# Optimization experiments

Hardware: AMD Instinct MI355X
Metric: run time of the kernel (lower is better)

The kernel has to match this reference:

```python
import jax, jax.numpy as jnp
import numpy as np

NU, NV, NF = 100000, 50000, 5000
D = 64
S, EUV = 5, 500000
EUF, EVF, EFU, EFV = 1000000, 500000, 1000000, 500000


def _spmm(rows, cols, vals, x, n_out):
    # COO sparse @ dense: out[r] += v * x[c]
    return jax.ops.segment_sum(vals[:, None] * x[cols], rows, num_segments=n_out)


def setup_inputs() -> dict:
    key = jax.random.key(0)
    ks = iter(jax.random.split(key, 32))
    f32 = jnp.float32
    inp = {
        'x_u': jax.random.normal(next(ks), (NU, D), f32),
        'x_v': jax.random.normal(next(ks), (NV, D), f32),
        'x_f': jax.random.normal(next(ks), (NF, D), f32),
    }
    for w in ['W_u_uv', 'W_v_uv', 'W_f2u', 'W_f2v', 'W_u2f', 'W_v2f']:
        inp[w] = jax.random.normal(next(ks), (D, D), f32) * (1.0 / np.sqrt(D))
    def edges(name, shape, n_row, n_col):
        inp[name + '_rows'] = jax.random.randint(next(ks), shape, 0, n_row, jnp.int32)
        inp[name + '_cols'] = jax.random.randint(next(ks), shape, 0, n_col, jnp.int32)
        inp[name + '_vals'] = jax.random.uniform(next(ks), shape, f32)
    edges('uv', (S, EUV), NU, NV)
    edges('vu', (S, EUV), NV, NU)
    edges('uf', (EUF,), NU, NF)
    edges('vf', (EVF,), NV, NF)
    edges('fu', (EFU,), NF, NU)
    edges('fv', (EFV,), NF, NV)
    return inp


def reference(x_u, x_v, x_f, W_u_uv, W_v_uv, W_f2u, W_f2v, W_u2f, W_v2f,
              uv_rows, uv_cols, uv_vals, vu_rows, vu_cols, vu_vals,
              uf_rows, uf_cols, uf_vals, vf_rows, vf_cols, vf_vals,
              fu_rows, fu_cols, fu_vals, fv_rows, fv_cols, fv_vals):
    nu, nv, nf = x_u.shape[0], x_v.shape[0], x_f.shape[0]
    # dense feature transforms (dropout=0 -> identity)
    u2f = x_u @ W_u2f
    v2f = x_v @ W_v2f
    f2u = x_f @ W_f2u
    f2v = x_f @ W_f2v
    tmp_u = x_u @ W_u_uv
    tmp_v = x_v @ W_v_uv
    # sum over rating supports == one segment_sum over flattened edges
    msg_u = _spmm(uv_rows.reshape(-1), uv_cols.reshape(-1), uv_vals.reshape(-1), tmp_v, nu)
    msg_v = _spmm(vu_rows.reshape(-1), vu_cols.reshape(-1), vu_vals.reshape(-1), tmp_u, nv)
    msg_u = msg_u + _spmm(uf_rows, uf_cols, uf_vals, f2u, nu)
    msg_v = msg_v + _spmm(vf_rows, vf_cols, vf_vals, f2v, nv)
    msg_f = _spmm(fu_rows, fu_cols, fu_vals, u2f, nf) + _spmm(fv_rows, fv_cols, fv_vals, v2f, nf)
    return jax.nn.relu(msg_u), jax.nn.relu(msg_v), jax.nn.relu(msg_f)
```

## Files before the change

kernel.cpp:

```cpp
#include <hip/hip_runtime.h>


#define TDIM 64
#define EPB  4096
#define STCAP 10240

struct Rel {
    const int* rows; const int* cols; const float* vals;
    int n, chunk0, boff, shift, srcflag, eoff, coladd;
};
struct RelPack { Rel r[6]; };

struct TPack {
    const float* X[3]; const float* W1[3]; const float* W2[3];
    unsigned short* Y1[3]; unsigned short* Y2[3];
    int N[3]; int c0[3];
};

struct FSPack {
    int c0A[3], cntA[3], offA[3];
    int c0B[3], cntB[3], offB[3];
};

struct GatherPack {
    const unsigned* srcA[3]; const unsigned* srcB[3];
    int n0, n1;
};

__device__ __forceinline__ unsigned short f2bf(float f) {
    union { float f; unsigned u; } c; c.f = f;
    unsigned r = c.u + 0x7FFFu + ((c.u >> 16) & 1u);
    return (unsigned short)(r >> 16);
}
__device__ __forceinline__ float bflo(unsigned x) { return __uint_as_float(x << 16); }
__device__ __forceinline__ float bfhi(unsigned x) { return __uint_as_float(x & 0xFFFF0000u); }
__device__ __forceinline__ float pval(unsigned p) {
    return __uint_as_float((p & 0x7FFFu) << 16);
}

__global__ __launch_bounds__(256) void transform_fused_kernel(TPack T)
{
    __shared__ float xsT[64 * 68];
    __shared__ float w1s[64 * 64];
    __shared__ float w2s[64 * 64];

    int t = 0;
    if ((int)blockIdx.x >= T.c0[1]) t = 1;
    if ((int)blockIdx.x >= T.c0[2]) t = 2;
    const float* __restrict__ X  = T.X[t];
    const float* __restrict__ W1 = T.W1[t];
    const float* __restrict__ W2 = T.W2[t];
    unsigned short* __restrict__ Y1 = T.Y1[t];
    unsigned short* __restrict__ Y2 = T.Y2[t];
    const int N    = T.N[t];
    const int row0 = (blockIdx.x - T.c0[t]) * 64;
    const int tid  = threadIdx.x;

    for (int i = tid * 4; i < 4096; i += 256 * 4) {
        *(float4*)&w1s[i] = *(const float4*)&W1[i];
        *(float4*)&w2s[i] = *(const float4*)&W2[i];
    }
    {
        const int r  = tid >> 2;
        const int c0 = (tid & 3) * 16;
        const int gr = row0 + r;
        #pragma unroll
        for (int cc = 0; cc < 16; cc += 4) {
            const int c = c0 + cc;
            float4 v = make_float4(0.f, 0.f, 0.f, 0.f);
            if (gr < N) v = *(const float4*)&X[(size_t)gr * TDIM + c];
            xsT[(c + 0) * 68 + r] = v.x;
            xsT[(c + 1) * 68 + r] = v.y;
            xsT[(c + 2) * 68 + r] = v.z;
            xsT[(c + 3) * 68 + r] = v.w;
        }
    }
    __syncthreads();

    const int tx = tid & 15;
    const int ty = tid >> 4;
    float a1[4][4] = {{0.f}}, a2[4][4] = {{0.f}};

    #pragma unroll 8
    for (int k = 0; k < 64; ++k) {
        const float4 xv = *(const float4*)&xsT[k * 68 + ty * 4];
        const float4 w1 = *(const float4*)&w1s[k * 64 + tx * 4];
        const float4 w2 = *(const float4*)&w2s[k * 64 + tx * 4];
        const float xr[4] = {xv.x, xv.y, xv.z, xv.w};
        const float c1[4] = {w1.x, w1.y, w1.z, w1.w};
        const float c2[4] = {w2.x, w2.y, w2.z, w2.w};
        #pragma unroll
        for (int r = 0; r < 4; ++r)
            #pragma unroll
            for (int c = 0; c < 4; ++c) {
                a1[r][c] = fmaf(xr[r], c1[c], a1[r][c]);
                a2[r][c] = fmaf(xr[r], c2[c], a2[r][c]);
            }
    }
    #pragma unroll
    for (int r = 0; r < 4; ++r) {
        const int gr = row0 + ty * 4 + r;
        if (gr < N) {
            ushort4 o1, o2;
            o1.x = f2bf(a1[r][0]); o1.y = f2bf(a1[r][1]);
            o1.z = f2bf(a1[r][2]); o1.w = f2bf(a1[r][3]);
            o2.x = f2bf(a2[r][0]); o2.y = f2bf(a2[r][1]);
            o2.z = f2bf(a2[r][2]); o2.w = f2bf(a2[r][3]);
            ((ushort4*)Y1)[(size_t)gr * 16 + tx] = o1;
            ((ushort4*)Y2)[(size_t)gr * 16 + tx] = o2;
        }
    }
}

__device__ __forceinline__ int find_rel(const RelPack& P, int chunk) {
    int ri = 0;
    if (chunk >= P.r[1].chunk0) ri = 1;
    if (chunk >= P.r[2].chunk0) ri = 2;
    if (chunk >= P.r[3].chunk0) ri = 3;
    if (chunk >= P.r[4].chunk0) ri = 4;
    if (chunk >= P.r[5].chunk0) ri = 5;
    return ri;
}

__global__ __launch_bounds__(512) void bucketize_cm_kernel(
    RelPack P, unsigned* __restrict__ pay, unsigned char* __restrict__ binb,
    int* __restrict__ localStart, int* __restrict__ bucketTotal, int NB)
{
    __shared__ int cnt[1536];
    __shared__ int sh[512];
    __shared__ unsigned stage_pay[EPB];
    __shared__ unsigned char stage_bin[EPB];

    const int tid   = threadIdx.x;
    const int chunk = blockIdx.x;
    for (int t = tid; t < NB; t += 512) cnt[t] = 0;
    __syncthreads();

    const int ri = find_rel(P, chunk);
    const Rel M = P.r[ri];
    const int i0    = (chunk - M.chunk0) * EPB;
    const int rbase = M.eoff + i0;
    const int count = min(EPB, M.n - i0);

    const int mask = (1 << M.shift) - 1;
    const unsigned sf = (unsigned)M.srcflag;

    int      m_[EPB / 512];
    unsigned x_[EPB / 512];
    #pragma unroll
    for (int k = 0; k < EPB / 512; ++k) {
        const int i = i0 + tid + k * 512;
        m_[k] = -1;
        if (i < M.n) {
            const int row = M.rows[i];
            const int b   = M.boff + (row >> M.shift);
            m_[k] = (b << 8) | (row & mask);
            x_[k] = (unsigned)M.cols[i] + (unsigned)M.coladd;
            atomicAdd(&cnt[b], 1);
        }
    }
    __syncthreads();

    int myv[3]; int lsum = 0;
    #pragma unroll
    for (int j = 0; j < 3; ++j) {
        const int idx = tid * 3 + j;
        myv[j] = (idx < NB) ? cnt[idx] : 0;
        lsum += myv[j];
    }
    sh[tid] = lsum;
    __syncthreads();
    for (int off = 1; off < 512; off <<= 1) {
        const int x = (tid >= off) ? sh[tid - off] : 0;
        __syncthreads();
        sh[tid] += x;
        __syncthreads();
    }
    int prefix = tid ? sh[tid - 1] : 0;
    const size_t lb = (size_t)chunk * (NB + 1);
    #pragma unroll
    for (int j = 0; j < 3; ++j) {
        const int idx = tid * 3 + j;
        if (idx < NB) {
            localStart[lb + idx] = prefix;
            if (myv[j]) atomicAdd(&bucketTotal[idx], myv[j]);
            cnt[idx] = prefix;
        } else if (idx == NB) {
            localStart[lb + NB] = prefix;
        }
        prefix += myv[j];
    }
    __syncthreads();

    #pragma unroll
    for (int k = 0; k < EPB / 512; ++k) {
        if (m_[k] >= 0) {
            const int i   = i0 + tid + k * 512;
            const int b   = m_[k] >> 8;
            const int pos = atomicAdd(&cnt[b], 1);
            stage_pay[pos] = (x_[k] << 15) | ((unsigned)f2bf(M.vals[i]) & 0x7FFFu);
            stage_bin[pos] = (unsigned char)(((m_[k] & 255) << 1) | sf);
        }
    }
    __syncthreads();

    #pragma unroll
    for (int k = 0; k < EPB / 512; ++k) {
        const int j = tid + k * 512;
        if (j < count) pay[rbase + j] = stage_pay[j];
    }
    {
        const int nfull = count >> 2;
        unsigned* bout = (unsigned*)(binb + rbase);
        const unsigned* bsrc = (const unsigned*)stage_bin;
        for (int j = tid; j < nfull; j += 512) bout[j] = bsrc[j];
        if (tid < (count & 3)) binb[rbase + nfull * 4 + tid] = stage_bin[nfull * 4 + tid];
    }
}

__global__ __launch_bounds__(256) void transpose_ls_kernel(
    const int* __restrict__ src, int* __restrict__ dst, int rows, int cols)
{
    __shared__ int tile[32][33];
    const int c0 = blockIdx.x * 32;
    const int r0 = blockIdx.y * 32;
    const int tx = threadIdx.x & 31;
    const int ty = threadIdx.x >> 5;
    #pragma unroll
    for (int k = 0; k < 32; k += 8) {
        const int r = r0 + ty + k, c = c0 + tx;
        if (r < rows && c < cols) tile[ty + k][tx] = src[(size_t)r * cols + c];
    }
    __syncthreads();
    #pragma unroll
    for (int k = 0; k < 32; k += 8) {
        const int c = c0 + ty + k, r = r0 + tx;
        if (c < cols && r < rows) dst[(size_t)c * rows + r] = tile[tx][ty + k];
    }
}

__global__ __launch_bounds__(256) void bscan_kernel(
    const int* __restrict__ bucketTotal, int* __restrict__ bbase, int NB)
{
    __shared__ int sh[256];
    __shared__ int carry;
    const int t = threadIdx.x;
    if (t == 0) carry = 0;
    __syncthreads();
    for (int b0 = 0; b0 < NB; b0 += 256) {
        const int idx = b0 + t;
        const int c = (idx < NB) ? bucketTotal[idx] : 0;
        sh[t] = c;
        __syncthreads();
        for (int off = 1; off < 256; off <<= 1) {
            const int x = (t >= off) ? sh[t - off] : 0;
            __syncthreads();
            sh[t] += x;
            __syncthreads();
        }
        const int cbase = carry;
        if (idx < NB) bbase[idx] = cbase + sh[t] - c;
        __syncthreads();
        if (t == 0) carry = cbase + sh[255];
        __syncthreads();
    }
    if (t == 0) bbase[NB] = carry;
}

__global__ __launch_bounds__(512) void finesort_kernel(
    const unsigned* __restrict__ pay, const unsigned char* __restrict__ binb,
    const int* __restrict__ TL, const int* __restrict__ bbase,
    FSPack F, int* __restrict__ p2, unsigned* __restrict__ arena,
    int nbU, int nbV, int NU, int NV, int NF, int NB, int ntot_rows,
    int nchunksTot)
{
    __shared__ int cnt[512];
    __shared__ int sh[512];
    __shared__ int runS[1024], runE[1024];
    __shared__ unsigned stage[STCAP];

    const int b   = blockIdx.x;
    const int tid = threadIdx.x;

    int t, lb, rowbase;
    if (b < nbU)              { t = 0; lb = b;              rowbase = 0; }
    else if (b < nbU + nbV)   { t = 1; lb = b - nbU;        rowbase = NU; }
    else                      { t = 2; lb = b - nbU - nbV;  rowbase = NU + NV; }
    const int shift     = (t == 2) ? 5 : 7;
    const int Ntype     = (t == 0) ? NU : (t == 1) ? NV : NF;
    const int row_start = lb << shift;
    const int nrows     = min(1 << shift, Ntype - row_start);
    const int nbins     = (1 << shift) * 2;
    const int grow0     = rowbase + row_start;

    const int nA = F.cntA[t], nB_ = F.cntB[t];
    const int nRuns = nA + nB_;

    const int* __restrict__ TLb  = TL + (size_t)b * nchunksTot;
    const int* __restrict__ TLb1 = TL + (size_t)(b + 1) * nchunksTot;
    for (int i = tid; i < nRuns; i += 512) {
        int ci, base;
        if (i < nA) { ci = F.c0A[t] + i;        base = F.offA[t] + i * EPB; }
        else        { int k = i - nA;
                      ci = F.c0B[t] + k;        base = F.offB[t] + k * EPB; }
        runS[i] = base + TLb[ci];
        runE[i] = base + TLb1[ci];
    }
    if (tid < nbins) cnt[tid] = 0;
    __syncthreads();

    const int s = bbase[b];
    const int e = bbase[b + 1];
    const bool staged = (e - s) <= STCAP;
    const int grp = tid >> 4;
    const int gl  = tid & 15;

    for (int ridx = grp; ridx < nRuns; ridx += 32) {
        const int rs = runS[ridx], re = runE[ridx];
        for (int j = rs + gl; j < re; j += 16) {
            atomicAdd(&cnt[binb[j]], 1);
        }
    }
    __syncthreads();

    const int v = (tid < nbins) ? cnt[tid] : 0;
    sh[tid] = v;
    __syncthreads();
    for (int off = 1; off < 512; off <<= 1) {
        const int x = (tid >= off) ? sh[tid - off] : 0;
        __syncthreads();
        sh[tid] += x;
        __syncthreads();
    }
    const int excl = sh[tid] - v;
    if (tid < nbins) cnt[tid] = staged ? excl : (s + excl);
    if (tid < nrows * 2) p2[2 * grow0 + tid] = s + excl;
    if (b == NB - 1 && tid == 0) p2[2 * ntot_rows] = e;
    __syncthreads();

    if (staged) {
        for (int ridx = grp; ridx < nRuns; ridx += 32) {
            const int rs = runS[ridx], re = runE[ridx];
            for (int j = rs + gl; j < re; j += 16) {
                const int pos = atomicAdd(&cnt[binb[j]], 1);
                stage[pos] = pay[j];
            }
        }
        __syncthreads();
        const int seglen = e - s;
        for (int j = tid; j < seglen; j += 512) arena[s + j] = stage[j];
    } else {
        for (int ridx = grp; ridx < nRuns; ridx += 32) {
            const int rs = runS[ridx], re = runE[ridx];
            for (int j = rs + gl; j < re; j += 16) {
                const int pos = atomicAdd(&cnt[binb[j]], 1);
                arena[pos] = pay[j];
            }
        }
    }
}

__device__ __forceinline__ void accum_seg(
    const unsigned* __restrict__ src, const unsigned* __restrict__ arena,
    const int s, const int e, const int g, const int li4,
    float (&acc)[8])
{
    if (s >= e) return;
    const int nb = (e - s + 7) >> 3;
    const unsigned* __restrict__ srcp = src + li4;

    unsigned x0[4], x1[4], x2[4], x3[4];
    float w0, w1, w2, w3;

    auto issue = [&](int j, unsigned* x, float& w) {
        const int idx = j + g;
        const bool ok = idx < e;
        const unsigned cv = arena[ok ? idx : s];
        w = ok ? pval(cv) : 0.f;
        const uint4 xv = *(const uint4*)&srcp[(cv >> 15) * 32u];
        x[0] = xv.x; x[1] = xv.y; x[2] = xv.z; x[3] = xv.w;
    };
    auto fmab = [&](const unsigned* x, float w) {
        #pragma unroll
        for (int q = 0; q < 4; ++q) {
            acc[2 * q]     = fmaf(w, bflo(x[q]), acc[2 * q]);
            acc[2 * q + 1] = fmaf(w, bfhi(x[q]), acc[2 * q + 1]);
        }
    };

    issue(s,      x0, w0);
    issue(s + 8,  x1, w1);
    issue(s + 16, x2, w2);
    issue(s + 24, x3, w3);
    __builtin_amdgcn_sched_barrier(0);

    int k = 0;
    for (;;) {
        fmab(x0, w0);
        if (k + 4 < nb) issue(s + (k + 4) * 8, x0, w0);
        __builtin_amdgcn_sched_barrier(0);
        if (++k >= nb) break;
        fmab(x1, w1);
        if (k + 4 < nb) issue(s + (k + 4) * 8, x1, w1);
        __builtin_amdgcn_sched_barrier(0);
        if (++k >= nb) break;
        fmab(x2, w2);
        if (k + 4 < nb) issue(s + (k + 4) * 8, x2, w2);
        __builtin_amdgcn_sched_barrier(0);
        if (++k >= nb) break;
        fmab(x3, w3);
        if (k + 4 < nb) issue(s + (k + 4) * 8, x3, w3);
        __builtin_amdgcn_sched_barrier(0);
        if (++k >= nb) break;
    }
}

__global__ __launch_bounds__(256) void gather_all_kernel(
    const int* __restrict__ p2, const unsigned* __restrict__ arena,
    GatherPack G, float* __restrict__ out, int nrow_total)
{
    const int gid  = (blockIdx.x * 256 + threadIdx.x) >> 6;
    const int lane = threadIdx.x & 63;
    const int g    = lane >> 3;
    const int li   = lane & 7;
    const int li4  = li * 4;
    if (gid >= nrow_total) return;
    const int wid = nrow_total - 1 - gid;

    int seg = 0;
    if (wid >= G.n1)      seg = 2;
    else if (wid >= G.n0) seg = 1;
    seg = __builtin_amdgcn_readfirstlane(seg);

    const int pa = __builtin_amdgcn_readfirstlane(p2[2 * wid]);
    const int pe = __builtin_amdgcn_readfirstlane(p2[2 * wid + 2]);

    float acc[8];
    #pragma unroll
    for (int k = 0; k < 8; ++k) acc[k] = 0.f;

    if (seg < 2) {
        accum_seg(G.srcA[seg], arena, pa, pe, g, li4, acc);
    } else {
        const int pm = __builtin_amdgcn_readfirstlane(p2[2 * wid + 1]);
        accum_seg(G.srcA[2], arena, pa, pm, g, li4, acc);
        accum_seg(G.srcB[2], arena, pm, pe, g, li4, acc);
    }

    #pragma unroll
    for (int k = 0; k < 8; ++k) {
        acc[k] += __shfl_xor(acc[k], 8, 64);
        acc[k] += __shfl_xor(acc[k], 16, 64);
        acc[k] += __shfl_xor(acc[k], 32, 64);
    }

    if (g == 0) {
        float4 o0, o1;
        o0.x = fmaxf(acc[0], 0.f); o0.y = fmaxf(acc[1], 0.f);
        o0.z = fmaxf(acc[2], 0.f); o0.w = fmaxf(acc[3], 0.f);
        o1.x = fmaxf(acc[4], 0.f); o1.y = fmaxf(acc[5], 0.f);
        o1.z = fmaxf(acc[6], 0.f); o1.w = fmaxf(acc[7], 0.f);
        float4* dst = (float4*)(out + (size_t)wid * 64 + li * 8);
        dst[0] = o0;
        dst[1] = o1;
    }
}

extern "C" void kernel_launch(void* const* d_in, const int* in_sizes, int n_in,
                              void* d_out, int out_size, void* d_ws, size_t ws_size,
                              hipStream_t stream)
{
    const float* x_u    = (const float*)d_in[0];
    const float* x_v    = (const float*)d_in[1];
    const float* x_f    = (const float*)d_in[2];
    const float* W_u_uv = (const float*)d_in[3];
    const float* W_v_uv = (const float*)d_in[4];
    const float* W_f2u  = (const float*)d_in[5];
    const float* W_f2v  = (const float*)d_in[6];
    const float* W_u2f  = (const float*)d_in[7];
    const float* W_v2f  = (const float*)d_in[8];

    const int* rows_[6] = {(const int*)d_in[9],  (const int*)d_in[12],
                           (const int*)d_in[15], (const int*)d_in[18],
                           (const int*)d_in[21], (const int*)d_in[24]};
    const int* cols_[6] = {(const int*)d_in[10], (const int*)d_in[13],
                           (const int*)d_in[16], (const int*)d_in[19],
                           (const int*)d_in[22], (const int*)d_in[25]};
    const float* vals_[6] = {(const float*)d_in[11], (const float*)d_in[14],
                             (const float*)d_in[17], (const float*)d_in[20],
                             (const float*)d_in[23], (const float*)d_in[26]};

    const int NU = in_sizes[0] / TDIM;
    const int NV = in_sizes[1] / TDIM;
    const int NF = in_sizes[2] / TDIM;
    const int E_[6] = {in_sizes[9], in_sizes[12], in_sizes[15],
                       in_sizes[18], in_sizes[21], in_sizes[24]};

    const int nbU = (NU + 127) >> 7;
    const int nbV = (NV + 127) >> 7;
    const int nbF = (NF + 31) >> 5;
    const int NB  = nbU + nbV + nbF;
    const int ntot_rows = NU + NV + NF;

    const int boff_[6]   = {0, nbU, 0, nbU, nbU + nbV, nbU + nbV};
    const int shift_[6]  = {7, 7, 7, 7, 5, 5};
    const int sflag_[6]  = {0, 0, 1, 1, 0, 1};
    const int coladd_[6] = {0, 0, NV, NU, 0, 0};

    size_t etot = 0;
    int eoff_[6];
    for (int r = 0; r < 6; ++r) { eoff_[r] = (int)etot; etot += (size_t)E_[r]; }

    RelPack P;
    int nchunks = 0;
    int relchunks[6];
    for (int r = 0; r < 6; ++r) {
        P.r[r].rows = rows_[r]; P.r[r].cols = cols_[r]; P.r[r].vals = vals_[r];
        P.r[r].n = E_[r]; P.r[r].chunk0 = nchunks;
        P.r[r].boff = boff_[r]; P.r[r].shift = shift_[r]; P.r[r].srcflag = sflag_[r];
        P.r[r].eoff = eoff_[r]; P.r[r].coladd = coladd_[r];
        relchunks[r] = (E_[r] + EPB - 1) / EPB;
        nchunks += relchunks[r];
    }

    char* wsb = (char*)d_ws;
    size_t o = 0;
    auto alloc = [&](size_t bytes) {
        char* p = wsb + o;
        o = (o + bytes + 15) & ~(size_t)15;
        return p;
    };
    unsigned short* utab = (unsigned short*)alloc(((size_t)NV + NF) * TDIM * 2);
    unsigned short* vtab = (unsigned short*)alloc(((size_t)NU + NF) * TDIM * 2);
    unsigned short* u2f  = (unsigned short*)alloc((size_t)NU * TDIM * 2);
    unsigned short* v2f  = (unsigned short*)alloc((size_t)NV * TDIM * 2);
    unsigned short* tmp_v = utab;
    unsigned short* f2u   = utab + (size_t)NV * TDIM;
    unsigned short* tmp_u = vtab;
    unsigned short* f2v   = vtab + (size_t)NU * TDIM;
    int* localStart  = (int*)alloc((size_t)nchunks * (NB + 1) * 4);
    int* TL          = (int*)alloc((size_t)(NB + 1) * nchunks * 4);
    int* bucketTotal = (int*)alloc((size_t)NB * 4);
    int* bbase       = (int*)alloc((size_t)(NB + 1) * 4);
    int* p2          = (int*)alloc((size_t)(2 * ntot_rows + 1) * 4);
    unsigned* pay        = (unsigned*)alloc(etot * 4);
    unsigned char* binb  = (unsigned char*)alloc(etot);
    unsigned* arena      = (unsigned*)alloc(etot * 4);
    (void)ws_size;

    TPack T;
    T.X[0] = x_u; T.W1[0] = W_u_uv; T.W2[0] = W_u2f; T.Y1[0] = tmp_u; T.Y2[0] = u2f; T.N[0] = NU;
    T.X[1] = x_v; T.W1[1] = W_v_uv; T.W2[1] = W_v2f; T.Y1[1] = tmp_v; T.Y2[1] = v2f; T.N[1] = NV;
    T.X[2] = x_f; T.W1[2] = W_f2u;  T.W2[2] = W_f2v; T.Y1[2] = f2u;  T.Y2[2] = f2v; T.N[2] = NF;
    T.c0[0] = 0;
    T.c0[1] = (NU + 63) / 64;
    T.c0[2] = T.c0[1] + (NV + 63) / 64;
    const int tchunks = T.c0[2] + (NF + 63) / 64;
    transform_fused_kernel<<<tchunks, 256, 0, stream>>>(T);

    hipMemsetAsync(bucketTotal, 0, (size_t)NB * sizeof(int), stream);
    bucketize_cm_kernel<<<nchunks, 512, 0, stream>>>(P, pay, binb, localStart, bucketTotal, NB);
    bscan_kernel<<<1, 256, 0, stream>>>(bucketTotal, bbase, NB);
    {
        dim3 tgrid((NB + 1 + 31) / 32, (nchunks + 31) / 32);
        transpose_ls_kernel<<<tgrid, 256, 0, stream>>>(localStart, TL, nchunks, NB + 1);
    }

    FSPack F;
    const int Arel[3] = {0, 1, 4}, Brel[3] = {2, 3, 5};
    for (int t = 0; t < 3; ++t) {
        F.c0A[t] = P.r[Arel[t]].chunk0; F.cntA[t] = relchunks[Arel[t]]; F.offA[t] = eoff_[Arel[t]];
        F.c0B[t] = P.r[Brel[t]].chunk0; F.cntB[t] = relchunks[Brel[t]]; F.offB[t] = eoff_[Brel[t]];
    }
    finesort_kernel<<<NB, 512, 0, stream>>>(
        pay, binb, TL, bbase, F, p2, arena, nbU, nbV, NU, NV, NF, NB, ntot_rows, nchunks);

    GatherPack G;
    G.srcA[0] = (const unsigned*)utab;  G.srcB[0] = (const unsigned*)utab;
    G.srcA[1] = (const unsigned*)vtab;  G.srcB[1] = (const unsigned*)vtab;
    G.srcA[2] = (const unsigned*)u2f;   G.srcB[2] = (const unsigned*)v2f;
    G.n0 = NU; G.n1 = NU + NV;

    gather_all_kernel<<<(ntot_rows + 3) / 4, 256, 0, stream>>>(
        p2, arena, G, (float*)d_out, ntot_rows);
}
```

Measured before the change: 512.5 us.

## Shrink local-start tables to 16-bit, fuse bucket scan into transpose, retune finesort groups

Stores per-chunk bucket offsets as 16-bit values, since counts within a 4096-edge chunk fit, which halves the localStart/TL traffic in the bucketize, transpose and finesort kernels. The single-block bucket prefix scan is merged into block (0,0) of the transpose kernel to drop one launch. The payload packing moves into the first pass so the vals array is read once, and finesort now uses 4-lane groups over 128 runs instead of 16-lane groups over 32. The folded scan serialises work inside one transpose block, and the narrower groups change the memory access pattern of the sort.

```diff
diff --git a/kernel.cpp b/kernel.cpp
--- a/kernel.cpp
+++ b/kernel.cpp
@@ -124,7 +124,8 @@
 
 __global__ __launch_bounds__(512) void bucketize_cm_kernel(
     RelPack P, unsigned* __restrict__ pay, unsigned char* __restrict__ binb,
-    int* __restrict__ localStart, int* __restrict__ bucketTotal, int NB)
+    unsigned short* __restrict__ localStart, int* __restrict__ bucketTotal,
+    int NB)
 {
     __shared__ int cnt[1536];
     __shared__ int sh[512];
@@ -155,7 +156,8 @@
             const int row = M.rows[i];
             const int b   = M.boff + (row >> M.shift);
             m_[k] = (b << 8) | (row & mask);
-            x_[k] = (unsigned)M.cols[i] + (unsigned)M.coladd;
+            const unsigned colp = (unsigned)M.cols[i] + (unsigned)M.coladd;
+            x_[k] = (colp << 15) | ((unsigned)f2bf(M.vals[i]) & 0x7FFFu);
             atomicAdd(&cnt[b], 1);
         }
     }
@@ -182,11 +184,11 @@
     for (int j = 0; j < 3; ++j) {
         const int idx = tid * 3 + j;
         if (idx < NB) {
-            localStart[lb + idx] = prefix;
+            localStart[lb + idx] = (unsigned short)prefix;
             if (myv[j]) atomicAdd(&bucketTotal[idx], myv[j]);
             cnt[idx] = prefix;
         } else if (idx == NB) {
-            localStart[lb + NB] = prefix;
+            localStart[lb + NB] = (unsigned short)prefix;
         }
         prefix += myv[j];
     }
@@ -195,10 +197,9 @@
     #pragma unroll
     for (int k = 0; k < EPB / 512; ++k) {
         if (m_[k] >= 0) {
-            const int i   = i0 + tid + k * 512;
             const int b   = m_[k] >> 8;
             const int pos = atomicAdd(&cnt[b], 1);
-            stage_pay[pos] = (x_[k] << 15) | ((unsigned)f2bf(M.vals[i]) & 0x7FFFu);
+            stage_pay[pos] = x_[k];
             stage_bin[pos] = (unsigned char)(((m_[k] & 255) << 1) | sf);
         }
     }
@@ -218,14 +219,45 @@
     }
 }
 
-__global__ __launch_bounds__(256) void transpose_ls_kernel(
-    const int* __restrict__ src, int* __restrict__ dst, int rows, int cols)
-{
-    __shared__ int tile[32][33];
+__global__ __launch_bounds__(256) void bscan_transpose_kernel(
+    const int* __restrict__ bucketTotal, int* __restrict__ bbase, int NB,
+    const unsigned short* __restrict__ src, unsigned short* __restrict__ dst,
+    int rows, int cols)
+{
+    __shared__ int shb[256];
+    __shared__ int carry;
+    __shared__ unsigned short tile[32][33];
+
+    const int t = threadIdx.x;
+
+    if (blockIdx.x == 0 && blockIdx.y == 0) {
+        if (t == 0) carry = 0;
+        __syncthreads();
+        for (int b0 = 0; b0 < NB; b0 += 256) {
+            const int idx = b0 + t;
+            const int c = (idx < NB) ? bucketTotal[idx] : 0;
+            shb[t] = c;
+            __syncthreads();
+            for (int off = 1; off < 256; off <<= 1) {
+                const int x = (t >= off) ? shb[t - off] : 0;
+                __syncthreads();
+                shb[t] += x;
+                __syncthreads();
+            }
+            const int cbase = carry;
+            if (idx < NB) bbase[idx] = cbase + shb[t] - c;
+            __syncthreads();
+            if (t == 0) carry = cbase + shb[255];
+            __syncthreads();
+        }
+        if (t == 0) bbase[NB] = carry;
+        __syncthreads();
+    }
+
     const int c0 = blockIdx.x * 32;
     const int r0 = blockIdx.y * 32;
-    const int tx = threadIdx.x & 31;
-    const int ty = threadIdx.x >> 5;
+    const int tx = t & 31;
+    const int ty = t >> 5;
     #pragma unroll
     for (int k = 0; k < 32; k += 8) {
         const int r = r0 + ty + k, c = c0 + tx;
@@ -239,37 +271,9 @@
     }
 }
 
-__global__ __launch_bounds__(256) void bscan_kernel(
-    const int* __restrict__ bucketTotal, int* __restrict__ bbase, int NB)
-{
-    __shared__ int sh[256];
-    __shared__ int carry;
-    const int t = threadIdx.x;
-    if (t == 0) carry = 0;
-    __syncthreads();
-    for (int b0 = 0; b0 < NB; b0 += 256) {
-        const int idx = b0 + t;
-        const int c = (idx < NB) ? bucketTotal[idx] : 0;
-        sh[t] = c;
-        __syncthreads();
-        for (int off = 1; off < 256; off <<= 1) {
-            const int x = (t >= off) ? sh[t - off] : 0;
-            __syncthreads();
-            sh[t] += x;
-            __syncthreads();
-        }
-        const int cbase = carry;
-        if (idx < NB) bbase[idx] = cbase + sh[t] - c;
-        __syncthreads();
-        if (t == 0) carry = cbase + sh[255];
-        __syncthreads();
-    }
-    if (t == 0) bbase[NB] = carry;
-}
-
 __global__ __launch_bounds__(512) void finesort_kernel(
     const unsigned* __restrict__ pay, const unsigned char* __restrict__ binb,
-    const int* __restrict__ TL, const int* __restrict__ bbase,
+    const unsigned short* __restrict__ TL, const int* __restrict__ bbase,
     FSPack F, int* __restrict__ p2, unsigned* __restrict__ arena,
     int nbU, int nbV, int NU, int NV, int NF, int NB, int ntot_rows,
     int nchunksTot)
@@ -296,15 +300,15 @@
     const int nA = F.cntA[t], nB_ = F.cntB[t];
     const int nRuns = nA + nB_;
 
-    const int* __restrict__ TLb  = TL + (size_t)b * nchunksTot;
-    const int* __restrict__ TLb1 = TL + (size_t)(b + 1) * nchunksTot;
+    const unsigned short* __restrict__ TLb  = TL + (size_t)b * nchunksTot;
+    const unsigned short* __restrict__ TLb1 = TL + (size_t)(b + 1) * nchunksTot;
     for (int i = tid; i < nRuns; i += 512) {
         int ci, base;
         if (i < nA) { ci = F.c0A[t] + i;        base = F.offA[t] + i * EPB; }
         else        { int k = i - nA;
                       ci = F.c0B[t] + k;        base = F.offB[t] + k * EPB; }
-        runS[i] = base + TLb[ci];
-        runE[i] = base + TLb1[ci];
+        runS[i] = base + (int)TLb[ci];
+        runE[i] = base + (int)TLb1[ci];
     }
     if (tid < nbins) cnt[tid] = 0;
     __syncthreads();
@@ -312,12 +316,12 @@
     const int s = bbase[b];
     const int e = bbase[b + 1];
     const bool staged = (e - s) <= STCAP;
-    const int grp = tid >> 4;
-    const int gl  = tid & 15;
-
-    for (int ridx = grp; ridx < nRuns; ridx += 32) {
+    const int grp = tid >> 2;
+    const int gl  = tid & 3;
+
+    for (int ridx = grp; ridx < nRuns; ridx += 128) {
         const int rs = runS[ridx], re = runE[ridx];
-        for (int j = rs + gl; j < re; j += 16) {
+        for (int j = rs + gl; j < re; j += 4) {
             atomicAdd(&cnt[binb[j]], 1);
         }
     }
@@ -339,9 +343,9 @@
     __syncthreads();
 
     if (staged) {
-        for (int ridx = grp; ridx < nRuns; ridx += 32) {
+        for (int ridx = grp; ridx < nRuns; ridx += 128) {
             const int rs = runS[ridx], re = runE[ridx];
-            for (int j = rs + gl; j < re; j += 16) {
+            for (int j = rs + gl; j < re; j += 4) {
                 const int pos = atomicAdd(&cnt[binb[j]], 1);
                 stage[pos] = pay[j];
             }
@@ -350,9 +354,9 @@
         const int seglen = e - s;
         for (int j = tid; j < seglen; j += 512) arena[s + j] = stage[j];
     } else {
-        for (int ridx = grp; ridx < nRuns; ridx += 32) {
+        for (int ridx = grp; ridx < nRuns; ridx += 128) {
             const int rs = runS[ridx], re = runE[ridx];
-            for (int j = rs + gl; j < re; j += 16) {
+            for (int j = rs + gl; j < re; j += 4) {
                 const int pos = atomicAdd(&cnt[binb[j]], 1);
                 arena[pos] = pay[j];
             }
@@ -538,8 +542,8 @@
     unsigned short* f2u   = utab + (size_t)NV * TDIM;
     unsigned short* tmp_u = vtab;
     unsigned short* f2v   = vtab + (size_t)NU * TDIM;
-    int* localStart  = (int*)alloc((size_t)nchunks * (NB + 1) * 4);
-    int* TL          = (int*)alloc((size_t)(NB + 1) * nchunks * 4);
+    unsigned short* localStart16 = (unsigned short*)alloc((size_t)nchunks * (NB + 1) * 2);
+    unsigned short* TL16         = (unsigned short*)alloc((size_t)(NB + 1) * nchunks * 2);
     int* bucketTotal = (int*)alloc((size_t)NB * 4);
     int* bbase       = (int*)alloc((size_t)(NB + 1) * 4);
     int* p2          = (int*)alloc((size_t)(2 * ntot_rows + 1) * 4);
@@ -559,11 +563,11 @@
     transform_fused_kernel<<<tchunks, 256, 0, stream>>>(T);
 
     hipMemsetAsync(bucketTotal, 0, (size_t)NB * sizeof(int), stream);
-    bucketize_cm_kernel<<<nchunks, 512, 0, stream>>>(P, pay, binb, localStart, bucketTotal, NB);
-    bscan_kernel<<<1, 256, 0, stream>>>(bucketTotal, bbase, NB);
+    bucketize_cm_kernel<<<nchunks, 512, 0, stream>>>(P, pay, binb, localStart16, bucketTotal, NB);
     {
         dim3 tgrid((NB + 1 + 31) / 32, (nchunks + 31) / 32);
-        transpose_ls_kernel<<<tgrid, 256, 0, stream>>>(localStart, TL, nchunks, NB + 1);
+        bscan_transpose_kernel<<<tgrid, 256, 0, stream>>>(
+            bucketTotal, bbase, NB, localStart16, TL16, nchunks, NB + 1);
     }
 
     FSPack F;
@@ -573,7 +577,7 @@
         F.c0B[t] = P.r[Brel[t]].chunk0; F.cntB[t] = relchunks[Brel[t]]; F.offB[t] = eoff_[Brel[t]];
     }
     finesort_kernel<<<NB, 512, 0, stream>>>(
-        pay, binb, TL, bbase, F, p2, arena, nbU, nbV, NU, NV, NF, NB, ntot_rows, nchunks);
+        pay, binb, TL16, bbase, F, p2, arena, nbU, nbV, NU, NV, NF, NB, ntot_rows, nchunks);
 
     GatherPack G;
     G.srcA[0] = (const unsigned*)utab;  G.srcB[0] = (const unsigned*)utab;
```

Measured after the change: 500.8 us. 2.3% less time.
